# Performance work log

Measured on AMD Instinct MI355X. Metric: run time of the kernel, lower is better.

Reference implementation:

```python
import jax, jax.numpy as jnp
import numpy as np

B, NPG, DEG = 256, 128, 16          # graphs per side, nodes per graph, avg degree
N = B * NPG                          # 32768 nodes per side
E = N * DEG                          # 524288 edges per side
F_IN, F1, F2, F3 = 64, 128, 64, 32   # number_labels, filters_1..3
TN, BINS = 16, 16                    # tensor_neurons, bins


def setup_inputs() -> dict:
    key = jax.random.key(0)
    ks = jax.random.split(key, 24)

    def make_edges(k):
        # random edges, each constrained within its own graph block
        base = jax.random.randint(k, (2, E), 0, NPG)
        off = jnp.repeat(jnp.arange(B, dtype=jnp.int64) * NPG, NPG * DEG)
        return (base + off[None, :]).astype(jnp.int64)

    def w(k, shape, fan_in):
        return (jax.random.normal(k, shape, jnp.float32) / np.sqrt(fan_in)).astype(jnp.float32)

    batch = jnp.repeat(jnp.arange(B, dtype=jnp.int64), NPG)
    return {
        'x1': jax.random.normal(ks[0], (N, F_IN), jnp.float32),
        'edge_index_1': make_edges(ks[1]),
        'batch_1': batch,
        'x2': jax.random.normal(ks[2], (N, F_IN), jnp.float32),
        'edge_index_2': make_edges(ks[3]),
        'batch_2': batch,
        # GCN layer params
        'W1': w(ks[4], (F_IN, F1), F_IN), 'b1': jnp.zeros((F1,), jnp.float32),
        'W2': w(ks[5], (F1, F2), F1),     'b2': jnp.zeros((F2,), jnp.float32),
        'W3': w(ks[6], (F2, F3), F2),     'b3': jnp.zeros((F3,), jnp.float32),
        # attention pooling
        'attW': w(ks[7], (F3, F3), F3),
        # tensor network module
        'tW': w(ks[8], (F3, F3, TN), F3),
        'tblock': w(ks[9], (TN, 2 * F3), 2 * F3),
        'tbias': jnp.zeros((TN,), jnp.float32),
        # scoring MLP (feature_count = TN + BINS -> 16 -> 1)
        'sW1': w(ks[10], (TN + BINS, 16), TN + BINS), 'sb1': jnp.zeros((16,), jnp.float32),
        'sW2': w(ks[11], (16, 1), 16),                'sb2': jnp.zeros((1,), jnp.float32),
    }


def _gcn(x, W, b, src, dst):
    # PyG GCNConv: add self-loops, symmetric deg^-1/2 normalization, then scatter-add
    n = x.shape[0]
    loop = jnp.arange(n, dtype=src.dtype)
    s = jnp.concatenate([src, loop])
    d = jnp.concatenate([dst, loop])
    deg = jax.ops.segment_sum(jnp.ones_like(d, dtype=x.dtype), d, num_segments=n)
    dinv = jax.lax.rsqrt(jnp.maximum(deg, 1e-12))
    norm = dinv[s] * dinv[d]                      # [E+N]
    h = x @ W                                     # [N, Fout]
    out = jax.ops.segment_sum(norm[:, None] * h[s], d, num_segments=n)
    return out + b


def _histc(v):
    # torch.histc with bins=BINS, min=max=0 -> uses data min/max; last bin inclusive
    v = v.reshape(-1)
    lo, hi = v.min(), v.max()
    idx = jnp.floor((v - lo) / jnp.maximum(hi - lo, 1e-12) * BINS)
    idx = jnp.clip(idx, 0, BINS - 1).astype(jnp.int32)
    h = jax.ops.segment_sum(jnp.ones_like(v), idx, num_segments=BINS)
    return h / h.sum()


def reference(x1, edge_index_1, batch_1, x2, edge_index_2, batch_2,
              W1, b1, W2, b2, W3, b3, attW, tW, tblock, tbias,
              sW1, sb1, sW2, sb2):
    def conv_pass(x, ei):
        src, dst = ei[0], ei[1]
        h = jax.nn.relu(_gcn(x, W1, b1, src, dst))   # dropout inactive (eval)
        h = jax.nn.relu(_gcn(h, W2, b2, src, dst))
        return _gcn(h, W3, b3, src, dst)

    f1 = conv_pass(x1, edge_index_1)
    f2 = conv_pass(x2, edge_index_2)

    # to_dense_batch: equal-sized, batch-sorted graphs -> plain reshape, full masks
    d1 = f1.reshape(B, NPG, F3)
    d2 = f2.reshape(B, NPG, F3)

    # per-graph-pair similarity histogram (detached in original)
    scores = jnp.einsum('bnd,bmd->bnm', jax.lax.stop_gradient(d1), jax.lax.stop_gradient(d2))
    hist = jax.vmap(_histc)(jax.nn.sigmoid(scores))  # [B, BINS]

    # attention pooling (SimGNN AttentionModule)
    def attn_pool(d):
        ctx = jnp.tanh(jnp.mean(d @ attW, axis=1))             # [B, F3]
        att = jax.nn.sigmoid(jnp.einsum('bnd,bd->bn', d, ctx))  # [B, NPG]
        return jnp.einsum('bnd,bn->bd', d, att)                 # [B, F3]

    e1 = attn_pool(d1)
    e2 = attn_pool(d2)

    # tensor network scoring
    tensor_scores = jnp.einsum('bi,ijk,bj->bk', e1, tW, e2)
    block_scores = jnp.concatenate([e1, e2], axis=-1) @ tblock.T
    tnm = jax.nn.relu(tensor_scores + block_scores + tbias)      # [B, TN]

    feat = jnp.concatenate([tnm, hist], axis=1)                  # [B, TN+BINS]
    h = jax.nn.relu(feat @ sW1 + sb1)
    score = jax.nn.sigmoid(h @ sW2 + sb2)
    return score.squeeze(-1)                                     # [B]
```

## Files before the change

kernel.cpp:

```cpp
#include <hip/hip_runtime.h>
#include <hip/hip_bf16.h>
#include <hip/hip_fp16.h>

#define N_NODES 32768
#define N_EDGES 524288
#define NGRAPH  256
#define NPG     128
#define EPG     2048
#define F_IN    64
#define F1      128
#define F2      64
#define F3      32
#define TN      16
#define BINS    16

typedef _Float16 f16;
typedef _Float16 f16x8 __attribute__((ext_vector_type(8)));
typedef float    f32x4 __attribute__((ext_vector_type(4)));

__device__ __forceinline__ float sigmoidf(float x) { return 1.f / (1.f + expf(-x)); }

#define L_A    0
#define L_R1   34816
#define L_R2   69632
#define L_R3   88064
#define L_R4   106496
#define L_R5   123904
#define L_DT   128512
#define L_DINV 148992
#define POOLB  149504

#define SA  136
#define SB  72
#define SD  40

template<int N, int K, int AS, int BS, int OS, bool TRANS, bool RELU>
__device__ __forceinline__ void mfma_mm(const f16* __restrict__ A,
                                        const f16* __restrict__ B,
                                        const float* __restrict__ bias,
                                        f16* __restrict__ out, int tid) {
    const int wv = tid >> 6, lane = tid & 63;
    const int col = lane & 15, g = lane >> 4;
    const int rowa = wv * 16 + col;
    constexpr int NT = N / 16, KS = K / 32;
    f32x4 acc[NT];
#pragma unroll
    for (int nt = 0; nt < NT; ++nt) {
        const float b = bias ? bias[nt * 16 + col] : 0.f;
        acc[nt] = (f32x4){b, b, b, b};
    }
#pragma unroll
    for (int ks = 0; ks < KS; ++ks) {
        const f16x8 a = *(const f16x8*)&A[rowa * AS + ks * 32 + g * 8];
#pragma unroll
        for (int nt = 0; nt < NT; ++nt) {
            const f16x8 b = *(const f16x8*)&B[(nt * 16 + col) * BS + ks * 32 + g * 8];
            acc[nt] = __builtin_amdgcn_mfma_f32_16x16x32_f16(a, b, acc[nt], 0, 0, 0);
        }
    }
#pragma unroll
    for (int nt = 0; nt < NT; ++nt)
#pragma unroll
        for (int j = 0; j < 4; ++j) {
            float v = acc[nt][j];
            if (RELU) v = fmaxf(v, 0.f);
            const int r = wv * 16 + g * 4 + j, c = nt * 16 + col;
            if (TRANS) out[c * OS + r] = (f16)v;
            else       out[r * OS + c] = (f16)v;
        }
}

__global__ __launch_bounds__(512, 1) void genn_all(
    const float* __restrict__ x1, const int* __restrict__ ei1,
    const float* __restrict__ x2, const int* __restrict__ ei2,
    const float* __restrict__ W1, const float* __restrict__ b1,
    const float* __restrict__ W2, const float* __restrict__ b2,
    const float* __restrict__ W3, const float* __restrict__ b3,
    const float* __restrict__ attW, const float* __restrict__ tW,
    const float* __restrict__ tblk, const float* __restrict__ tbias,
    const float* __restrict__ sW1, const float* __restrict__ sb1,
    const float* __restrict__ sW2, const float* __restrict__ sb2,
    float* __restrict__ outp) {
    __shared__ __align__(16) char pool[POOLB];
    unsigned int* Acnt = (unsigned int*)(pool + L_A);
    f16*   Amat = (f16*)(pool + L_A);
    f16*   dts  = (f16*)(pool + L_DT);
    float* dinv = (float*)(pool + L_DINV);

    const int g = blockIdx.x;
    const int tid = threadIdx.x;
    const int wv = tid >> 6, lane = tid & 63;

    for (int side = 0; side < 2; ++side) {
        const float* xg = (side ? x2 : x1) + (size_t)g * NPG * F_IN;
        const int* eib  = side ? ei2 : ei1;
        const int* srcg = eib + (size_t)g * EPG;
        const int* dstg = eib + N_EDGES + (size_t)g * EPG;
        const int nb = g * NPG;

        for (int i = tid; i < 2176; i += 512)
            ((uint4*)Acnt)[i] = make_uint4(0, 0, 0, 0);
        __syncthreads();

#pragma unroll
        for (int it = 0; it < EPG / 512; ++it) {
            const int e = it * 512 + tid;
            const int d = dstg[e] - nb;
            const int s = srcg[e] - nb;
            atomicAdd(&Acnt[d * 68 + (s >> 1)], 1u << ((s & 1) << 4));
        }
        {
            f16* xT = (f16*)(pool + L_R1);
#pragma unroll
            for (int it = 0; it < 4; ++it) {
                const int idx = (it * 512 + tid) * 4;
                const float4 v = *(const float4*)&xg[idx];
                const int n = idx >> 6, c = idx & 63;
                xT[(c + 0) * SA + n] = (f16)v.x;
                xT[(c + 1) * SA + n] = (f16)v.y;
                xT[(c + 2) * SA + n] = (f16)v.z;
                xT[(c + 3) * SA + n] = (f16)v.w;
            }
            f16* W1T = (f16*)(pool + L_R2);
            for (int i = tid; i < F_IN * F1; i += 512)
                W1T[(i & 127) * SB + (i >> 7)] = (f16)W1[i];
            if (side == 0) {
                f16* W2T = (f16*)(pool + L_R4);
                for (int i = tid; i < F1 * F2; i += 512)
                    W2T[(i & 63) * SA + (i >> 6)] = (f16)W2[i];
                f16* W3T = (f16*)(pool + L_R5);
                for (int i = tid; i < F2 * F3; i += 512)
                    W3T[(i & 31) * SB + (i >> 5)] = (f16)W3[i];
            }
        }
        __syncthreads();

        {
            const int d = tid >> 2, q = tid & 3;
            unsigned int s = 0;
            const unsigned int* rp = &Acnt[d * 68 + q * 17];
            for (int j = 0; j < 17; ++j) {
                const unsigned int v = rp[j];
                s += (v & 0xffffu) + (v >> 16);
            }
            s += __shfl_down((int)s, 2);
            s += __shfl_down((int)s, 1);
            if (q == 0) dinv[d] = rsqrtf((float)s + 1.0f);
        }
        __syncthreads();

        for (int i = tid; i < 8704; i += 512) {
            const int d = i / 68, w = i % 68;
            const unsigned int v = Acnt[i];
            const int s0 = 2 * w, s1 = 2 * w + 1;
            int c0 = v & 0xffffu, c1 = v >> 16;
            if (s0 == d) ++c0;
            if (s1 == d) ++c1;
            const float dd = dinv[d];
            const f16 f0 = (f16)((float)c0 * dinv[s0 & 127] * dd);
            const f16 f1 = (f16)((float)c1 * dinv[s1 & 127] * dd);
            unsigned int o;
            unsigned short u0 = __builtin_bit_cast(unsigned short, f0);
            unsigned short u1 = __builtin_bit_cast(unsigned short, f1);
            o = (unsigned int)u0 | ((unsigned int)u1 << 16);
            Acnt[i] = o;
        }
        __syncthreads();

        f16* xT   = (f16*)(pool + L_R1);
        f16* h1   = (f16*)(pool + L_R1);
        f16* W1T  = (f16*)(pool + L_R2);
        f16* h2   = (f16*)(pool + L_R2);
        f16* out1 = (f16*)(pool + L_R3);
        f16* t2T  = (f16*)(pool + L_R3);
        f16* t3T  = (f16*)(pool + L_R3);
        f16* W2T  = (f16*)(pool + L_R4);
        f16* W3T  = (f16*)(pool + L_R5);

        mfma_mm<64, 128, SA, SA, SB, false, false>(Amat, xT, nullptr, out1, tid);
        __syncthreads();
        mfma_mm<128, 64, SB, SB, SA, false, true>(out1, W1T, b1, h1, tid);
        __syncthreads();
        mfma_mm<64, 128, SA, SA, SA, true, false>(h1, W2T, nullptr, t2T, tid);
        __syncthreads();
        mfma_mm<64, 128, SA, SA, SB, false, true>(Amat, t2T, b2, h2, tid);
        __syncthreads();
        mfma_mm<32, 64, SB, SB, SA, true, false>(h2, W3T, nullptr, t3T, tid);
        __syncthreads();
        mfma_mm<32, 128, SA, SA, SD, false, false>(Amat, t3T, b3,
                                                   dts + side * (NPG * SD), tid);
        __syncthreads();
    }

    unsigned short* lhist = (unsigned short*)(pool + L_R4);
    float* pf   = (float*)(pool + L_R3);
    float* red  = pf;
    float* lohi = pf + 16;
    float* meanv= pf + 18;
    float* ctxv = pf + 82;
    float* ev   = pf + 146;
    float* feat = pf + 210;
    float* hv   = pf + 242;
    float* av   = pf + 258;
    float* pmean= pf + 514;
    float* ptens= pf + 1026;
    int*   bins2= (int*)(pf + 1538);
    const f16* d1 = dts;
    const f16* d2 = dts + NPG * SD;

    const int col = lane & 15, gq = lane >> 4;
    const int rowa = wv * 16 + col;
    f32x4 acc[8];
#pragma unroll
    for (int nt = 0; nt < 8; ++nt) acc[nt] = (f32x4){0.f, 0.f, 0.f, 0.f};
    {
        const f16x8 a = *(const f16x8*)&d1[rowa * SD + gq * 8];
#pragma unroll
        for (int nt = 0; nt < 8; ++nt) {
            const f16x8 b = *(const f16x8*)&d2[(nt * 16 + col) * SD + gq * 8];
            acc[nt] = __builtin_amdgcn_mfma_f32_16x16x32_f16(a, b, acc[nt], 0, 0, 0);
        }
    }
    for (int i = tid; i < 4352; i += 512) ((unsigned int*)lhist)[i] = 0u;
    float lmin = acc[0][0], lmax = acc[0][0];
#pragma unroll
    for (int nt = 0; nt < 8; ++nt)
#pragma unroll
        for (int j = 0; j < 4; ++j) {
            lmin = fminf(lmin, acc[nt][j]);
            lmax = fmaxf(lmax, acc[nt][j]);
        }
    for (int off = 32; off; off >>= 1) {
        lmin = fminf(lmin, __shfl_down(lmin, off));
        lmax = fmaxf(lmax, __shfl_down(lmax, off));
    }
    if (lane == 0) { red[wv] = lmin; red[8 + wv] = lmax; }
    __syncthreads();
    if (tid == 0) {
        float mn = red[0], mx = red[8];
        for (int w = 1; w < 8; ++w) { mn = fminf(mn, red[w]); mx = fmaxf(mx, red[8 + w]); }
        lohi[0] = sigmoidf(mn);
        lohi[1] = sigmoidf(mx);
    }
    __syncthreads();
    const float lo = lohi[0];
    const float denom = fmaxf(lohi[1] - lo, 1e-12f);

    {
        unsigned short* lh = &lhist[tid * 17];
#pragma unroll
        for (int nt = 0; nt < 8; ++nt)
#pragma unroll
            for (int j = 0; j < 4; ++j) {
                const float v = sigmoidf(acc[nt][j]);
                int b = (int)floorf((v - lo) / denom * (float)BINS);
                b = min(max(b, 0), BINS - 1);
                lh[b]++;
            }
    }
    __syncthreads();
    if (tid < 256) {
        const int b = tid & 15, chunk = tid >> 4;
        int s = 0;
        for (int i = 0; i < 32; ++i) s += lhist[(chunk * 32 + i) * 17 + b];
        bins2[chunk * 16 + b] = s;
    }
    __syncthreads();

    {
        const int cc = tid & 63, chunk = tid >> 6;
        const int side = cc >> 5, c = cc & 31;
        const f16* dp = dts + side * (NPG * SD);
        float s = 0.f;
        const int nbs = chunk * 16;
        for (int n = 0; n < 16; ++n) s += (float)dp[(nbs + n) * SD + c];
        pmean[chunk * 64 + cc] = s;
    }
    __syncthreads();
    if (tid < 64) {
        float s = 0.f;
        for (int c = 0; c < 8; ++c) s += pmean[c * 64 + tid];
        meanv[tid] = s * (1.f / NPG);
    }
    __syncthreads();
    if (tid < 64) {
        const int c = tid & 31;
        const float* mv = &meanv[(tid >> 5) * 32];
        float a = 0.f;
        for (int k = 0; k < F3; ++k) a += mv[k] * attW[k * F3 + c];
        ctxv[tid] = tanhf(a);
    }
    __syncthreads();
    if (tid < 256) {
        const int n = tid & 127, side = tid >> 7;
        const f16* dp = dts + side * (NPG * SD);
        const float* cx = &ctxv[side * 32];
        float a = 0.f;
        for (int k = 0; k < F3; ++k) a += (float)dp[n * SD + k] * cx[k];
        av[tid] = sigmoidf(a);
    }
    __syncthreads();
    {
        const int cc = tid & 63, chunk = tid >> 6;
        const int side = cc >> 5, c = cc & 31;
        const f16* dp = dts + side * (NPG * SD);
        const float* a = &av[side * 128];
        float s = 0.f;
        const int nbs = chunk * 16;
        for (int n = 0; n < 16; ++n) s += a[nbs + n] * (float)dp[(nbs + n) * SD + c];
        pmean[chunk * 64 + cc] = s;
    }
    __syncthreads();
    if (tid < 64) {
        float s = 0.f;
        for (int c = 0; c < 8; ++c) s += pmean[c * 64 + tid];
        ev[tid] = s;
    }
    __syncthreads();

    {
        const int k = tid & 15, i = tid >> 4;
        const float e1i = ev[i];
        float a = 0.f;
        for (int j = 0; j < F3; ++j) a += ev[32 + j] * tW[(i * F3 + j) * TN + k];
        ptens[i * 16 + k] = e1i * a;
    }
    __syncthreads();
    if (tid < TN) {
        float a = tbias[tid];
        for (int i = 0; i < 32; ++i) a += ptens[i * 16 + tid];
        for (int i = 0; i < F3; ++i) a += ev[i] * tblk[tid * 2 * F3 + i];
        for (int j = 0; j < F3; ++j) a += ev[32 + j] * tblk[tid * 2 * F3 + F3 + j];
        feat[tid] = fmaxf(a, 0.f);
    } else if (tid < TN + BINS) {
        const int b = tid - TN;
        int s = 0;
        for (int c = 0; c < 16; ++c) s += bins2[c * 16 + b];
        feat[tid] = (float)s * (1.f / (NPG * NPG));
    }
    __syncthreads();
    if (tid < 16) {
        float a = sb1[tid];
        for (int i = 0; i < TN + BINS; ++i) a += feat[i] * sW1[i * 16 + tid];
        hv[tid] = fmaxf(a, 0.f);
    }
    __syncthreads();
    if (tid == 0) {
        float a = sb2[0];
        for (int j = 0; j < 16; ++j) a += hv[j] * sW2[j];
        outp[g] = sigmoidf(a);
    }
}

extern "C" void kernel_launch(void* const* d_in, const int* in_sizes, int n_in,
                              void* d_out, int out_size, void* d_ws, size_t ws_size,
                              hipStream_t stream) {
    const float* x1   = (const float*)d_in[0];
    const int*   ei1  = (const int*)d_in[1];
    const float* x2   = (const float*)d_in[3];
    const int*   ei2  = (const int*)d_in[4];
    const float* W1   = (const float*)d_in[6];
    const float* b1   = (const float*)d_in[7];
    const float* W2   = (const float*)d_in[8];
    const float* b2   = (const float*)d_in[9];
    const float* W3   = (const float*)d_in[10];
    const float* b3   = (const float*)d_in[11];
    const float* attW = (const float*)d_in[12];
    const float* tW   = (const float*)d_in[13];
    const float* tblk = (const float*)d_in[14];
    const float* tbias= (const float*)d_in[15];
    const float* sW1  = (const float*)d_in[16];
    const float* sb1  = (const float*)d_in[17];
    const float* sW2  = (const float*)d_in[18];
    const float* sb2  = (const float*)d_in[19];
    float* out = (float*)d_out;
    (void)in_sizes; (void)n_in; (void)out_size; (void)d_ws; (void)ws_size;

    genn_all<<<NGRAPH, 512, 0, stream>>>(x1, ei1, x2, ei2,
                                         W1, b1, W2, b2, W3, b3,
                                         attW, tW, tblk, tbias,
                                         sW1, sb1, sW2, sb2, out);
}
```

Measured before the change: 35.52 us.

## Double block size to 1024 threads, splitting MFMA column tiles across wave halves

Launches 1024 threads per graph block instead of 512. Each MFMA matmul is split so 16 waves share the work, with two waves per 16-row strip each taking half the column tiles. All strided loops and reductions are rescaled to match. The histogram now compares raw scores against 15 precomputed logit thresholds instead of taking a sigmoid and floor per element, uses byte counters, and transposed outputs are written as packed f16x4 stores. This targets per-block latency from the serial chain of small matmuls, at the cost of more register pressure and barrier overhead, and byte counters that could overflow if one thread ever counts 256 or more in a bin.

```diff
diff --git a/kernel.cpp b/kernel.cpp
--- a/kernel.cpp
+++ b/kernel.cpp
@@ -15,6 +15,7 @@
 #define BINS    16
 
 typedef _Float16 f16;
+typedef _Float16 f16x4 __attribute__((ext_vector_type(4)));
 typedef _Float16 f16x8 __attribute__((ext_vector_type(8)));
 typedef float    f32x4 __attribute__((ext_vector_type(4)));
 
@@ -39,38 +40,50 @@
                                         const f16* __restrict__ B,
                                         const float* __restrict__ bias,
                                         f16* __restrict__ out, int tid) {
-    const int wv = tid >> 6, lane = tid & 63;
+    const int w = tid >> 6, lane = tid & 63;
     const int col = lane & 15, g = lane >> 4;
-    const int rowa = wv * 16 + col;
-    constexpr int NT = N / 16, KS = K / 32;
-    f32x4 acc[NT];
-#pragma unroll
-    for (int nt = 0; nt < NT; ++nt) {
-        const float b = bias ? bias[nt * 16 + col] : 0.f;
+    const int strip = w & 7, nh = w >> 3;
+    const int rowa = strip * 16 + col;
+    constexpr int NT = N / 16, KS = K / 32, NT2 = NT / 2;
+    f32x4 acc[NT2];
+#pragma unroll
+    for (int nt = 0; nt < NT2; ++nt) {
+        const float b = bias ? bias[(nh * NT2 + nt) * 16 + col] : 0.f;
         acc[nt] = (f32x4){b, b, b, b};
     }
 #pragma unroll
     for (int ks = 0; ks < KS; ++ks) {
         const f16x8 a = *(const f16x8*)&A[rowa * AS + ks * 32 + g * 8];
 #pragma unroll
-        for (int nt = 0; nt < NT; ++nt) {
-            const f16x8 b = *(const f16x8*)&B[(nt * 16 + col) * BS + ks * 32 + g * 8];
+        for (int nt = 0; nt < NT2; ++nt) {
+            const f16x8 b = *(const f16x8*)&B[((nh * NT2 + nt) * 16 + col) * BS + ks * 32 + g * 8];
             acc[nt] = __builtin_amdgcn_mfma_f32_16x16x32_f16(a, b, acc[nt], 0, 0, 0);
         }
     }
 #pragma unroll
-    for (int nt = 0; nt < NT; ++nt)
-#pragma unroll
-        for (int j = 0; j < 4; ++j) {
-            float v = acc[nt][j];
-            if (RELU) v = fmaxf(v, 0.f);
-            const int r = wv * 16 + g * 4 + j, c = nt * 16 + col;
-            if (TRANS) out[c * OS + r] = (f16)v;
-            else       out[r * OS + c] = (f16)v;
-        }
+    for (int nt = 0; nt < NT2; ++nt) {
+        const int c = (nh * NT2 + nt) * 16 + col;
+        if (TRANS) {
+            f16x4 o;
+#pragma unroll
+            for (int j = 0; j < 4; ++j) {
+                float v = acc[nt][j];
+                if (RELU) v = fmaxf(v, 0.f);
+                o[j] = (f16)v;
+            }
+            *(f16x4*)&out[c * OS + strip * 16 + g * 4] = o;
+        } else {
+#pragma unroll
+            for (int j = 0; j < 4; ++j) {
+                float v = acc[nt][j];
+                if (RELU) v = fmaxf(v, 0.f);
+                out[(strip * 16 + g * 4 + j) * OS + c] = (f16)v;
+            }
+        }
+    }
 }
 
-__global__ __launch_bounds__(512, 1) void genn_all(
+__global__ __launch_bounds__(1024, 4) void genn_all(
     const float* __restrict__ x1, const int* __restrict__ ei1,
     const float* __restrict__ x2, const int* __restrict__ ei2,
     const float* __restrict__ W1, const float* __restrict__ b1,
@@ -98,13 +111,13 @@
         const int* dstg = eib + N_EDGES + (size_t)g * EPG;
         const int nb = g * NPG;
 
-        for (int i = tid; i < 2176; i += 512)
+        for (int i = tid; i < 2176; i += 1024)
             ((uint4*)Acnt)[i] = make_uint4(0, 0, 0, 0);
         __syncthreads();
 
 #pragma unroll
-        for (int it = 0; it < EPG / 512; ++it) {
-            const int e = it * 512 + tid;
+        for (int it = 0; it < EPG / 1024; ++it) {
+            const int e = it * 1024 + tid;
             const int d = dstg[e] - nb;
             const int s = srcg[e] - nb;
             atomicAdd(&Acnt[d * 68 + (s >> 1)], 1u << ((s & 1) << 4));
@@ -112,8 +125,8 @@
         {
             f16* xT = (f16*)(pool + L_R1);
 #pragma unroll
-            for (int it = 0; it < 4; ++it) {
-                const int idx = (it * 512 + tid) * 4;
+            for (int it = 0; it < 2; ++it) {
+                const int idx = (it * 1024 + tid) * 4;
                 const float4 v = *(const float4*)&xg[idx];
                 const int n = idx >> 6, c = idx & 63;
                 xT[(c + 0) * SA + n] = (f16)v.x;
@@ -122,20 +135,20 @@
                 xT[(c + 3) * SA + n] = (f16)v.w;
             }
             f16* W1T = (f16*)(pool + L_R2);
-            for (int i = tid; i < F_IN * F1; i += 512)
+            for (int i = tid; i < F_IN * F1; i += 1024)
                 W1T[(i & 127) * SB + (i >> 7)] = (f16)W1[i];
             if (side == 0) {
                 f16* W2T = (f16*)(pool + L_R4);
-                for (int i = tid; i < F1 * F2; i += 512)
+                for (int i = tid; i < F1 * F2; i += 1024)
                     W2T[(i & 63) * SA + (i >> 6)] = (f16)W2[i];
                 f16* W3T = (f16*)(pool + L_R5);
-                for (int i = tid; i < F2 * F3; i += 512)
+                for (int i = tid; i < F2 * F3; i += 1024)
                     W3T[(i & 31) * SB + (i >> 5)] = (f16)W3[i];
             }
         }
         __syncthreads();
 
-        {
+        if (tid < 512) {
             const int d = tid >> 2, q = tid & 3;
             unsigned int s = 0;
             const unsigned int* rp = &Acnt[d * 68 + q * 17];
@@ -149,7 +162,7 @@
         }
         __syncthreads();
 
-        for (int i = tid; i < 8704; i += 512) {
+        for (int i = tid; i < 8704; i += 1024) {
             const int d = i / 68, w = i % 68;
             const unsigned int v = Acnt[i];
             const int s0 = 2 * w, s1 = 2 * w + 1;
@@ -159,11 +172,9 @@
             const float dd = dinv[d];
             const f16 f0 = (f16)((float)c0 * dinv[s0 & 127] * dd);
             const f16 f1 = (f16)((float)c1 * dinv[s1 & 127] * dd);
-            unsigned int o;
             unsigned short u0 = __builtin_bit_cast(unsigned short, f0);
             unsigned short u1 = __builtin_bit_cast(unsigned short, f1);
-            o = (unsigned int)u0 | ((unsigned int)u1 << 16);
-            Acnt[i] = o;
+            Acnt[i] = (unsigned int)u0 | ((unsigned int)u1 << 16);
         }
         __syncthreads();
 
@@ -192,39 +203,41 @@
         __syncthreads();
     }
 
-    unsigned short* lhist = (unsigned short*)(pool + L_R4);
+    unsigned char* lhist = (unsigned char*)(pool + L_R4);
     float* pf   = (float*)(pool + L_R3);
     float* red  = pf;
-    float* lohi = pf + 16;
-    float* meanv= pf + 18;
-    float* ctxv = pf + 82;
-    float* ev   = pf + 146;
-    float* feat = pf + 210;
-    float* hv   = pf + 242;
-    float* av   = pf + 258;
-    float* pmean= pf + 514;
-    float* ptens= pf + 1026;
-    int*   bins2= (int*)(pf + 1538);
+    float* lohi = pf + 32;
+    float* meanv= pf + 34;
+    float* ctxv = pf + 98;
+    float* ev   = pf + 162;
+    float* feat = pf + 226;
+    float* hv   = pf + 258;
+    float* thr  = pf + 274;
+    float* av   = pf + 290;
+    float* pmean= pf + 546;
+    float* ptens= pf + 1570;
+    int*   bins2= (int*)(pf + 2082);
     const f16* d1 = dts;
     const f16* d2 = dts + NPG * SD;
 
     const int col = lane & 15, gq = lane >> 4;
-    const int rowa = wv * 16 + col;
-    f32x4 acc[8];
-#pragma unroll
-    for (int nt = 0; nt < 8; ++nt) acc[nt] = (f32x4){0.f, 0.f, 0.f, 0.f};
+    const int strip = wv & 7, nh = wv >> 3;
+    const int rowa = strip * 16 + col;
+    f32x4 acc[4];
+#pragma unroll
+    for (int nt = 0; nt < 4; ++nt) acc[nt] = (f32x4){0.f, 0.f, 0.f, 0.f};
     {
         const f16x8 a = *(const f16x8*)&d1[rowa * SD + gq * 8];
 #pragma unroll
-        for (int nt = 0; nt < 8; ++nt) {
-            const f16x8 b = *(const f16x8*)&d2[(nt * 16 + col) * SD + gq * 8];
+        for (int nt = 0; nt < 4; ++nt) {
+            const f16x8 b = *(const f16x8*)&d2[((nh * 4 + nt) * 16 + col) * SD + gq * 8];
             acc[nt] = __builtin_amdgcn_mfma_f32_16x16x32_f16(a, b, acc[nt], 0, 0, 0);
         }
     }
-    for (int i = tid; i < 4352; i += 512) ((unsigned int*)lhist)[i] = 0u;
+    for (int i = tid; i < 4352; i += 1024) ((unsigned int*)lhist)[i] = 0u;
     float lmin = acc[0][0], lmax = acc[0][0];
 #pragma unroll
-    for (int nt = 0; nt < 8; ++nt)
+    for (int nt = 0; nt < 4; ++nt)
 #pragma unroll
         for (int j = 0; j < 4; ++j) {
             lmin = fminf(lmin, acc[nt][j]);
@@ -234,27 +247,33 @@
         lmin = fminf(lmin, __shfl_down(lmin, off));
         lmax = fmaxf(lmax, __shfl_down(lmax, off));
     }
-    if (lane == 0) { red[wv] = lmin; red[8 + wv] = lmax; }
+    if (lane == 0) { red[wv] = lmin; red[16 + wv] = lmax; }
     __syncthreads();
     if (tid == 0) {
-        float mn = red[0], mx = red[8];
-        for (int w = 1; w < 8; ++w) { mn = fminf(mn, red[w]); mx = fmaxf(mx, red[8 + w]); }
-        lohi[0] = sigmoidf(mn);
-        lohi[1] = sigmoidf(mx);
-    }
-    __syncthreads();
-    const float lo = lohi[0];
-    const float denom = fmaxf(lohi[1] - lo, 1e-12f);
+        float mn = red[0], mx = red[16];
+        for (int w = 1; w < 16; ++w) { mn = fminf(mn, red[w]); mx = fmaxf(mx, red[16 + w]); }
+        const float los = sigmoidf(mn);
+        const float den = fmaxf(sigmoidf(mx) - los, 1e-12f);
+        lohi[0] = los;
+        lohi[1] = den;
+    }
+    __syncthreads();
+    if (tid < 15) {
+        const float p = lohi[0] + (float)(tid + 1) * lohi[1] * (1.f / 16.f);
+        thr[tid] = logf(p / (1.f - p));
+    }
+    __syncthreads();
 
     {
-        unsigned short* lh = &lhist[tid * 17];
-#pragma unroll
-        for (int nt = 0; nt < 8; ++nt)
+        unsigned char* lh = &lhist[tid * 17];
+#pragma unroll
+        for (int nt = 0; nt < 4; ++nt)
 #pragma unroll
             for (int j = 0; j < 4; ++j) {
-                const float v = sigmoidf(acc[nt][j]);
-                int b = (int)floorf((v - lo) / denom * (float)BINS);
-                b = min(max(b, 0), BINS - 1);
+                const float x = acc[nt][j];
+                int b = 0;
+#pragma unroll
+                for (int k = 0; k < 15; ++k) b += (x >= thr[k]) ? 1 : 0;
                 lh[b]++;
             }
     }
@@ -262,7 +281,7 @@
     if (tid < 256) {
         const int b = tid & 15, chunk = tid >> 4;
         int s = 0;
-        for (int i = 0; i < 32; ++i) s += lhist[(chunk * 32 + i) * 17 + b];
+        for (int i = 0; i < 64; ++i) s += lhist[(chunk * 64 + i) * 17 + b];
         bins2[chunk * 16 + b] = s;
     }
     __syncthreads();
@@ -272,14 +291,14 @@
         const int side = cc >> 5, c = cc & 31;
         const f16* dp = dts + side * (NPG * SD);
         float s = 0.f;
-        const int nbs = chunk * 16;
-        for (int n = 0; n < 16; ++n) s += (float)dp[(nbs + n) * SD + c];
+        const int nbs = chunk * 8;
+        for (int n = 0; n < 8; ++n) s += (float)dp[(nbs + n) * SD + c];
         pmean[chunk * 64 + cc] = s;
     }
     __syncthreads();
     if (tid < 64) {
         float s = 0.f;
-        for (int c = 0; c < 8; ++c) s += pmean[c * 64 + tid];
+        for (int c = 0; c < 16; ++c) s += pmean[c * 64 + tid];
         meanv[tid] = s * (1.f / NPG);
     }
     __syncthreads();
@@ -306,19 +325,19 @@
         const f16* dp = dts + side * (NPG * SD);
         const float* a = &av[side * 128];
         float s = 0.f;
-        const int nbs = chunk * 16;
-        for (int n = 0; n < 16; ++n) s += a[nbs + n] * (float)dp[(nbs + n) * SD + c];
+        const int nbs = chunk * 8;
+        for (int n = 0; n < 8; ++n) s += a[nbs + n] * (float)dp[(nbs + n) * SD + c];
         pmean[chunk * 64 + cc] = s;
     }
     __syncthreads();
     if (tid < 64) {
         float s = 0.f;
-        for (int c = 0; c < 8; ++c) s += pmean[c * 64 + tid];
+        for (int c = 0; c < 16; ++c) s += pmean[c * 64 + tid];
         ev[tid] = s;
     }
     __syncthreads();
 
-    {
+    if (tid < 512) {
         const int k = tid & 15, i = tid >> 4;
         const float e1i = ev[i];
         float a = 0.f;
@@ -376,8 +395,8 @@
     float* out = (float*)d_out;
     (void)in_sizes; (void)n_in; (void)out_size; (void)d_ws; (void)ws_size;
 
-    genn_all<<<NGRAPH, 512, 0, stream>>>(x1, ei1, x2, ei2,
-                                         W1, b1, W2, b2, W3, b3,
-                                         attW, tW, tblk, tbias,
-                                         sW1, sb1, sW2, sb2, out);
+    genn_all<<<NGRAPH, 1024, 0, stream>>>(x1, ei1, x2, ei2,
+                                          W1, b1, W2, b2, W3, b3,
+                                          attW, tW, tblk, tbias,
+                                          sW1, sb1, sW2, sb2, out);
 }
```

Measured after the change: 34.87 us, median of 2. No clear change (-1.8%).
